# Optimization experiments

Hardware: AMD Instinct MI355X
Metric: run time of the kernel (lower is better)

## Reference

```python
import jax, jax.numpy as jnp
import numpy as np

B, D = 32, 2048


def setup_inputs() -> dict:
    key = jax.random.key(0)
    ks = jax.random.split(key, 7)
    # torch init: weights ~ N(0, 0.1^2); biases default Linear uniform(-1/sqrt(D), 1/sqrt(D))
    bound = 1.0 / np.sqrt(D)
    return {
        "x": jax.random.normal(ks[0], (B, D), dtype=jnp.float32),
        "Wq": 0.1 * jax.random.normal(ks[1], (D, D), dtype=jnp.float32),
        "bq": jax.random.uniform(ks[2], (D,), minval=-bound, maxval=bound, dtype=jnp.float32),
        "Wk": 0.1 * jax.random.normal(ks[3], (D, D), dtype=jnp.float32),
        "bk": jax.random.uniform(ks[4], (D,), minval=-bound, maxval=bound, dtype=jnp.float32),
        "Wv": 0.1 * jax.random.normal(ks[5], (D, D), dtype=jnp.float32),
        "bv": jax.random.uniform(ks[6], (D,), minval=-bound, maxval=bound, dtype=jnp.float32),
    }


def reference(x, Wq, bq, Wk, bk, Wv, bv):
    # q,k,v: [B, D] feature-wise projections (torch Linear: x @ W^T + b)
    q = x @ Wq.T + bq
    k = x @ Wk.T + bk
    v = x @ Wv.T + bv
    # rank-1 outer product scores[b,i,j] = q[b,i] * k[b,j]  -> [B, D, D]
    scores = q[:, :, None] * k[:, None, :]
    # softmax over dim=1 (as in the original F.softmax(..., dim=1))
    weights = jax.nn.softmax(scores, axis=1)
    # weighted V sum: out[b,i] = sum_j weights[b,i,j] * v[b,j]  -> [B, D]
    out = jnp.einsum("bij,bj->bi", weights, v)
    return out
```

## Files before the change

### kernel.cpp

```cpp
#include <hip/hip_runtime.h>
#include <math.h>


#define D 2048
#define BATCH 32
#define CAP 2080
#define WIN8 260

#define Q_OFF   0
#define K2_OFF  65536
#define V_OFF   131072
#define Z_OFF   196608
#define CNT_OFF 262144
#define MM_OFF  262208
#define KDP_OFF 262272
#define XH_OFF  395392
#define XL_OFF  428160

#define L2E 1.4426950408889634f

typedef short s16x8 __attribute__((ext_vector_type(8)));
typedef float f32x4 __attribute__((ext_vector_type(4)));
typedef unsigned short u16;

union FragU { s16x8 v; unsigned u[4]; };

__device__ __forceinline__ float fast_exp2(float x) {
#if __has_builtin(__builtin_amdgcn_exp2f)
  return __builtin_amdgcn_exp2f(x);
#else
  return exp2f(x);
#endif
}
__device__ __forceinline__ u16 f2bf(float f) {
  unsigned u = __float_as_uint(f);
  u = u + 0x7FFFu + ((u >> 16) & 1u);
  return (u16)(u >> 16);
}
__device__ __forceinline__ float bf2f(u16 h) {
  return __uint_as_float(((unsigned)h) << 16);
}
__device__ __forceinline__ void cvt2(float a, float b, unsigned& hp,
                                     unsigned& lp) {
  unsigned ua = __float_as_uint(a), ub = __float_as_uint(b);
  unsigned ha = ua & 0xFFFF0000u, hb = ub & 0xFFFF0000u;
  float la = a - __uint_as_float(ha);
  float lb = b - __uint_as_float(hb);
  hp = (ua >> 16) | hb;
  lp = (__float_as_uint(la) >> 16) | (__float_as_uint(lb) & 0xFFFF0000u);
}

__global__ __launch_bounds__(256) void k0_init(
    const float* __restrict__ x,
    const float* __restrict__ bq, const float* __restrict__ bk,
    const float* __restrict__ bv, float* __restrict__ ws,
    float* __restrict__ out) {
  const int bx = blockIdx.x, tid = threadIdx.x;
  if (bx < 768) {
    const int g = bx * 256 + tid;
    const int m = g >> 16, i = g & 2047;
    ws[g] = (m == 0) ? bq[i] : (m == 1) ? bk[i] * L2E : bv[i];
  } else if (bx < 832) {
    const int idx = (bx - 768) * 256 + tid;
    float4 v = ((const float4*)x)[idx];
    u16* xh = (u16*)(ws + XH_OFF);
    u16* xl = (u16*)(ws + XL_OFF);
    u16 h0 = f2bf(v.x), h1 = f2bf(v.y), h2 = f2bf(v.z), h3 = f2bf(v.w);
    ushort4 hh = {h0, h1, h2, h3};
    ushort4 ll = {f2bf(v.x - bf2f(h0)), f2bf(v.y - bf2f(h1)),
                  f2bf(v.z - bf2f(h2)), f2bf(v.w - bf2f(h3))};
    *(ushort4*)(xh + idx * 4) = hh;
    *(ushort4*)(xl + idx * 4) = ll;
  } else if (bx < 1089) {
    const int g = (bx - 832) * 256 + tid;
    if (g < 65600) ws[Z_OFF + g] = 0.f;
  } else if (bx < 1153) {
    const int idx = (bx - 1089) * 256 + tid;
    ((float4*)out)[idx] = make_float4(0.f, 0.f, 0.f, 0.f);
  } else {
    const int idx = (bx - 1153) * 256 + tid;
    ((float2*)(ws + KDP_OFF))[idx] = make_float2(0.f, -1e30f);
  }
}

__global__ __launch_bounds__(256, 3) void k1_proj(
    const float* __restrict__ Wq, const float* __restrict__ Wk,
    const float* __restrict__ Wv, float* __restrict__ ws) {
  __shared__ float red[4][512];
  const int tid = threadIdx.x;
  const int lane = tid & 63, wv = tid >> 6;
  const int tile = blockIdx.x >> 1, kh = blockIdx.x & 1;
  const int r0 = tile * 16;
  const int m = r0 >> 11, lr = r0 & 2047;
  const float* W = (m == 0) ? Wq : (m == 1) ? Wk : Wv;
  const u16* xh = (const u16*)(ws + XH_OFF);
  const u16* xl = (const u16*)(ws + XL_OFF);

  const int kbase = kh * 1024 + wv * 256 + (lane >> 4) * 8;
  const float* ap = W + (size_t)(lr + (lane & 15)) * D + kbase;
  const u16* bh0 = xh + (size_t)(lane & 15) * D + kbase;
  const u16* bl0 = xl + (size_t)(lane & 15) * D + kbase;
  const u16* bh1 = bh0 + 16 * D;
  const u16* bl1 = bl0 + 16 * D;

  f32x4 acc0 = {0.f, 0.f, 0.f, 0.f}, acc1 = {0.f, 0.f, 0.f, 0.f};
#pragma unroll
  for (int s = 0; s < 8; ++s) {
    float4 fa = *(const float4*)(ap + s * 32);
    float4 fb = *(const float4*)(ap + s * 32 + 4);
    s16x8 Bh0 = *(const s16x8*)(bh0 + s * 32);
    s16x8 Bl0 = *(const s16x8*)(bl0 + s * 32);
    s16x8 Bh1 = *(const s16x8*)(bh1 + s * 32);
    s16x8 Bl1 = *(const s16x8*)(bl1 + s * 32);
    FragU Ah, Al;
    cvt2(fa.x, fa.y, Ah.u[0], Al.u[0]);
    cvt2(fa.z, fa.w, Ah.u[1], Al.u[1]);
    cvt2(fb.x, fb.y, Ah.u[2], Al.u[2]);
    cvt2(fb.z, fb.w, Ah.u[3], Al.u[3]);
    acc0 = __builtin_amdgcn_mfma_f32_16x16x32_bf16(Ah.v, Bh0, acc0, 0, 0, 0);
    acc1 = __builtin_amdgcn_mfma_f32_16x16x32_bf16(Ah.v, Bh1, acc1, 0, 0, 0);
    acc0 = __builtin_amdgcn_mfma_f32_16x16x32_bf16(Ah.v, Bl0, acc0, 0, 0, 0);
    acc1 = __builtin_amdgcn_mfma_f32_16x16x32_bf16(Ah.v, Bl1, acc1, 0, 0, 0);
    acc0 = __builtin_amdgcn_mfma_f32_16x16x32_bf16(Al.v, Bh0, acc0, 0, 0, 0);
    acc1 = __builtin_amdgcn_mfma_f32_16x16x32_bf16(Al.v, Bh1, acc1, 0, 0, 0);
  }
  const int col = lane & 15, rq = (lane >> 4) * 4;
#pragma unroll
  for (int r = 0; r < 4; ++r) {
    red[wv][col * 16 + rq + r] = acc0[r];
    red[wv][(col + 16) * 16 + rq + r] = acc1[r];
  }
  __syncthreads();
  const float scale = (m == 1) ? L2E : 1.0f;
#pragma unroll
  for (int i = tid; i < 512; i += 256) {
    float s = ((red[0][i] + red[1][i]) + (red[2][i] + red[3][i])) * scale;
    atomicAdd(ws + (size_t)m * 65536 + (size_t)(i >> 4) * D + lr + (i & 15), s);
  }
}

__global__ __launch_bounds__(256) void k2_minmax(float* __restrict__ ws) {
  const int b = blockIdx.x, tid = threadIdx.x;
  const float* q = ws + Q_OFF + (size_t)b * D;
  float mx = -1e30f, mn = 1e30f;
  for (int i = tid; i < D / 4; i += 256) {
    float4 v = *(const float4*)(q + i * 4);
    mx = fmaxf(mx, fmaxf(fmaxf(v.x, v.y), fmaxf(v.z, v.w)));
    mn = fminf(mn, fminf(fminf(v.x, v.y), fminf(v.z, v.w)));
  }
#pragma unroll
  for (int off = 32; off; off >>= 1) {
    mx = fmaxf(mx, __shfl_down(mx, off));
    mn = fminf(mn, __shfl_down(mn, off));
  }
  __shared__ float smx[4], smn[4];
  if ((tid & 63) == 0) { smx[tid >> 6] = mx; smn[tid >> 6] = mn; }
  __syncthreads();
  if (tid == 0) {
    mx = fmaxf(fmaxf(smx[0], smx[1]), fmaxf(smx[2], smx[3]));
    mn = fminf(fminf(smn[0], smn[1]), fminf(smn[2], smn[3]));
    ws[MM_OFF + b] = mx;
    ws[MM_OFF + 32 + b] = mn;
  }
}

__global__ __launch_bounds__(256, 8) void k3_denom(float* __restrict__ ws) {
  __shared__ float qs[256];
  const int bx = blockIdx.x, tid = threadIdx.x;
  const int b = bx >> 6, rem = bx & 63, jc = rem >> 3, ih = rem & 7;
  if (tid < 64)
    *(float4*)&qs[tid * 4] =
        *(const float4*)(ws + Q_OFF + (size_t)b * D + ih * 256 + tid * 4);
  __syncthreads();

  const int j = jc * 256 + tid;
  const float k2 = ws[K2_OFF + (size_t)b * D + j];
  const float qmax = ws[MM_OFF + b], qmin = ws[MM_OFF + 32 + b];
  const float m2 = (k2 >= 0.f) ? k2 * qmax : k2 * qmin;
  const float nm2 = -m2;
  float z0 = 0.f, z1 = 0.f, z2 = 0.f, z3 = 0.f;
#pragma unroll 4
  for (int i = 0; i < 256; i += 4) {
    float4 qv = *(const float4*)&qs[i];
    z0 += fast_exp2(fmaf(qv.x, k2, nm2));
    z1 += fast_exp2(fmaf(qv.y, k2, nm2));
    z2 += fast_exp2(fmaf(qv.z, k2, nm2));
    z3 += fast_exp2(fmaf(qv.w, k2, nm2));
  }
  atomicAdd(ws + Z_OFF + (size_t)b * D + j, (z0 + z1) + (z2 + z3));
}

__global__ __launch_bounds__(256) void k3b_finalize(float* __restrict__ ws) {
  const int bx = blockIdx.x;
  const int b = bx >> 3;
  const int j = (bx & 7) * 256 + threadIdx.x;
  const size_t o = (size_t)b * D + j;
  const float k2 = ws[K2_OFF + o];
  const float Z = ws[Z_OFF + o];
  const float v = ws[V_OFF + o];
  const float qmax = ws[MM_OFF + b], qmin = ws[MM_OFF + 32 + b];
  const float m2 = (k2 >= 0.f) ? k2 * qmax : k2 * qmin;
  const float d = __log2f(fabsf(v) / Z) - m2;
  int* cnt = (int*)(ws + CNT_OFF);
  int slot;
  if (v >= 0.f) slot = atomicAdd(&cnt[b], 1);
  else          slot = CAP - 1 - atomicAdd(&cnt[32 + b], 1);
  float2* kdp = (float2*)(ws + KDP_OFF) + (size_t)b * CAP;
  kdp[slot] = make_float2(k2, d);
}

__global__ __launch_bounds__(256, 8) void k4_out(const float* __restrict__ ws,
                                                 float* __restrict__ out) {
  __shared__ float kd[WIN8 * 2];
  const int bx = blockIdx.x, tid = threadIdx.x;
  const int b = bx >> 6, rem = bx & 63, ic = rem >> 3, jw = rem & 7;
  const int w0 = jw * WIN8;
  const float* src = ws + KDP_OFF + (size_t)b * (CAP * 2) + (size_t)w0 * 2;
  if (tid < (WIN8 * 2) / 4)
    *(float4*)&kd[tid * 4] = *(const float4*)(src + tid * 4);
  const int npos = ((const int*)(ws + CNT_OFF))[b];
  __syncthreads();

  const int i = ic * 256 + tid;
  const float qi = ws[Q_OFF + (size_t)b * D + i];

  const int posEnd = (npos + 7) & ~7;
  const int negStart = (CAP - (D - npos)) & ~7;
  int aHi = min(posEnd, w0 + WIN8) - w0; if (aHi < 0) aHi = 0;
  int bLo = max(negStart, w0) - w0;      if (bLo > WIN8) bLo = WIN8;

  float p0 = 0.f, p1 = 0.f, p2 = 0.f, p3 = 0.f;
  for (int jj = 0; jj < aHi; jj += 4) {
    float4 t0 = *(const float4*)&kd[jj * 2];
    float4 t1 = *(const float4*)&kd[jj * 2 + 4];
    p0 += fast_exp2(fmaf(qi, t0.x, t0.y));
    p1 += fast_exp2(fmaf(qi, t0.z, t0.w));
    p2 += fast_exp2(fmaf(qi, t1.x, t1.y));
    p3 += fast_exp2(fmaf(qi, t1.z, t1.w));
  }
  float n0 = 0.f, n1 = 0.f, n2 = 0.f, n3 = 0.f;
  for (int jj = bLo; jj < WIN8; jj += 4) {
    float4 t0 = *(const float4*)&kd[jj * 2];
    float4 t1 = *(const float4*)&kd[jj * 2 + 4];
    n0 += fast_exp2(fmaf(qi, t0.x, t0.y));
    n1 += fast_exp2(fmaf(qi, t0.z, t0.w));
    n2 += fast_exp2(fmaf(qi, t1.x, t1.y));
    n3 += fast_exp2(fmaf(qi, t1.z, t1.w));
  }
  float res = ((p0 + p1) + (p2 + p3)) - ((n0 + n1) + (n2 + n3));
  atomicAdd(out + (size_t)b * D + i, res);
}

extern "C" void kernel_launch(void* const* d_in, const int* in_sizes, int n_in,
                              void* d_out, int out_size, void* d_ws, size_t ws_size,
                              hipStream_t stream) {
  (void)in_sizes; (void)n_in; (void)out_size; (void)ws_size;
  const float* x  = (const float*)d_in[0];
  const float* Wq = (const float*)d_in[1];
  const float* bq = (const float*)d_in[2];
  const float* Wk = (const float*)d_in[3];
  const float* bk = (const float*)d_in[4];
  const float* Wv = (const float*)d_in[5];
  const float* bv = (const float*)d_in[6];
  float* ws  = (float*)d_ws;
  float* out = (float*)d_out;

  k0_init<<<1413, 256, 0, stream>>>(x, bq, bk, bv, ws, out);
  k1_proj<<<768, 256, 0, stream>>>(Wq, Wk, Wv, ws);
  k2_minmax<<<BATCH, 256, 0, stream>>>(ws);
  k3_denom<<<2048, 256, 0, stream>>>(ws);
  k3b_finalize<<<256, 256, 0, stream>>>(ws);
  k4_out<<<2048, 256, 0, stream>>>(ws, out);
}
```

Measured before the change: 159.6 us.

## Fuse minmax, denominator and finalize into one kernel; drop atomics via split partial buffers

The projection now writes its two K-halves into separate partial buffers instead of atomically accumulating onto bias-initialized outputs. Bias add, q min/max, the softmax denominator and the sign-partitioned (k,d) packing are fused into a single per-(batch, j-chunk) kernel that uses block-local counters and per-segment padding. The output kernel processes all 8 segments per block and reduces in shared memory, so out no longer needs zero-init or atomics. This removes several launches, the init kernel's clears and global atomics, at the cost of fewer, larger blocks (256 per kernel) and a full 1024-length q sweep per thread.

```diff
diff --git a/kernel.cpp b/kernel.cpp
--- a/kernel.cpp
+++ b/kernel.cpp
@@ -4,18 +4,14 @@
 
 #define D 2048
 #define BATCH 32
-#define CAP 2080
-#define WIN8 260
-
-#define Q_OFF   0
-#define K2_OFF  65536
-#define V_OFF   131072
-#define Z_OFF   196608
-#define CNT_OFF 262144
-#define MM_OFF  262208
-#define KDP_OFF 262272
-#define XH_OFF  395392
-#define XL_OFF  428160
+#define SEG 260
+
+#define XH_OFF  0
+#define XL_OFF  32768
+#define PA_OFF  65536
+#define PB_OFF  262144
+#define KDP_OFF 458752
+#define NP_OFF  591872
 
 #define L2E 1.4426950408889634f
 
@@ -50,37 +46,18 @@
   lp = (__float_as_uint(la) >> 16) | (__float_as_uint(lb) & 0xFFFF0000u);
 }
 
-__global__ __launch_bounds__(256) void k0_init(
-    const float* __restrict__ x,
-    const float* __restrict__ bq, const float* __restrict__ bk,
-    const float* __restrict__ bv, float* __restrict__ ws,
-    float* __restrict__ out) {
-  const int bx = blockIdx.x, tid = threadIdx.x;
-  if (bx < 768) {
-    const int g = bx * 256 + tid;
-    const int m = g >> 16, i = g & 2047;
-    ws[g] = (m == 0) ? bq[i] : (m == 1) ? bk[i] * L2E : bv[i];
-  } else if (bx < 832) {
-    const int idx = (bx - 768) * 256 + tid;
-    float4 v = ((const float4*)x)[idx];
-    u16* xh = (u16*)(ws + XH_OFF);
-    u16* xl = (u16*)(ws + XL_OFF);
-    u16 h0 = f2bf(v.x), h1 = f2bf(v.y), h2 = f2bf(v.z), h3 = f2bf(v.w);
-    ushort4 hh = {h0, h1, h2, h3};
-    ushort4 ll = {f2bf(v.x - bf2f(h0)), f2bf(v.y - bf2f(h1)),
-                  f2bf(v.z - bf2f(h2)), f2bf(v.w - bf2f(h3))};
-    *(ushort4*)(xh + idx * 4) = hh;
-    *(ushort4*)(xl + idx * 4) = ll;
-  } else if (bx < 1089) {
-    const int g = (bx - 832) * 256 + tid;
-    if (g < 65600) ws[Z_OFF + g] = 0.f;
-  } else if (bx < 1153) {
-    const int idx = (bx - 1089) * 256 + tid;
-    ((float4*)out)[idx] = make_float4(0.f, 0.f, 0.f, 0.f);
-  } else {
-    const int idx = (bx - 1153) * 256 + tid;
-    ((float2*)(ws + KDP_OFF))[idx] = make_float2(0.f, -1e30f);
-  }
+__global__ __launch_bounds__(64) void k0_cvt(const float* __restrict__ x,
+                                             float* __restrict__ ws) {
+  const int idx = blockIdx.x * 64 + threadIdx.x;
+  float4 v = ((const float4*)x)[idx];
+  u16* xh = (u16*)(ws + XH_OFF);
+  u16* xl = (u16*)(ws + XL_OFF);
+  u16 h0 = f2bf(v.x), h1 = f2bf(v.y), h2 = f2bf(v.z), h3 = f2bf(v.w);
+  ushort4 hh = {h0, h1, h2, h3};
+  ushort4 ll = {f2bf(v.x - bf2f(h0)), f2bf(v.y - bf2f(h1)),
+                f2bf(v.z - bf2f(h2)), f2bf(v.w - bf2f(h3))};
+  *(ushort4*)(xh + idx * 4) = hh;
+  *(ushort4*)(xl + idx * 4) = ll;
 }
 
 __global__ __launch_bounds__(256, 3) void k1_proj(
@@ -131,124 +108,136 @@
     red[wv][(col + 16) * 16 + rq + r] = acc1[r];
   }
   __syncthreads();
-  const float scale = (m == 1) ? L2E : 1.0f;
+  float* part = ws + (kh ? PB_OFF : PA_OFF) + (size_t)m * 65536;
 #pragma unroll
   for (int i = tid; i < 512; i += 256) {
-    float s = ((red[0][i] + red[1][i]) + (red[2][i] + red[3][i])) * scale;
-    atomicAdd(ws + (size_t)m * 65536 + (size_t)(i >> 4) * D + lr + (i & 15), s);
-  }
-}
-
-__global__ __launch_bounds__(256) void k2_minmax(float* __restrict__ ws) {
-  const int b = blockIdx.x, tid = threadIdx.x;
-  const float* q = ws + Q_OFF + (size_t)b * D;
-  float mx = -1e30f, mn = 1e30f;
-  for (int i = tid; i < D / 4; i += 256) {
-    float4 v = *(const float4*)(q + i * 4);
-    mx = fmaxf(mx, fmaxf(fmaxf(v.x, v.y), fmaxf(v.z, v.w)));
-    mn = fminf(mn, fminf(fminf(v.x, v.y), fminf(v.z, v.w)));
-  }
+    float s = (red[0][i] + red[1][i]) + (red[2][i] + red[3][i]);
+    part[(size_t)(i >> 4) * D + lr + (i & 15)] = s;
+  }
+}
+
+__global__ __launch_bounds__(512) void k3_dz(float* __restrict__ ws,
+                                             const float* __restrict__ bq,
+                                             const float* __restrict__ bk,
+                                             const float* __restrict__ bv) {
+  __shared__ float qs[2048];
+  __shared__ float zs[512];
+  __shared__ float rmx[8], rmn[8];
+  __shared__ int cnt[2];
+  const int bx = blockIdx.x, t = threadIdx.x;
+  const int b = bx >> 3, jc = bx & 7;
+  if (t == 0) { cnt[0] = 0; cnt[1] = 0; }
+
+  const float* qA = ws + PA_OFF + (size_t)b * D;
+  const float* qB = ws + PB_OFF + (size_t)b * D;
+  float4 a4 = ((const float4*)qA)[t];
+  float4 b4 = ((const float4*)qB)[t];
+  float4 c4 = ((const float4*)bq)[t];
+  float4 qv = {a4.x + b4.x + c4.x, a4.y + b4.y + c4.y,
+               a4.z + b4.z + c4.z, a4.w + b4.w + c4.w};
+  *(float4*)&qs[t * 4] = qv;
+  float mx = fmaxf(fmaxf(qv.x, qv.y), fmaxf(qv.z, qv.w));
+  float mn = fminf(fminf(qv.x, qv.y), fminf(qv.z, qv.w));
 #pragma unroll
   for (int off = 32; off; off >>= 1) {
     mx = fmaxf(mx, __shfl_down(mx, off));
     mn = fminf(mn, __shfl_down(mn, off));
   }
-  __shared__ float smx[4], smn[4];
-  if ((tid & 63) == 0) { smx[tid >> 6] = mx; smn[tid >> 6] = mn; }
-  __syncthreads();
-  if (tid == 0) {
-    mx = fmaxf(fmaxf(smx[0], smx[1]), fmaxf(smx[2], smx[3]));
-    mn = fminf(fminf(smn[0], smn[1]), fminf(smn[2], smn[3]));
-    ws[MM_OFF + b] = mx;
-    ws[MM_OFF + 32 + b] = mn;
-  }
-}
-
-__global__ __launch_bounds__(256, 8) void k3_denom(float* __restrict__ ws) {
-  __shared__ float qs[256];
-  const int bx = blockIdx.x, tid = threadIdx.x;
-  const int b = bx >> 6, rem = bx & 63, jc = rem >> 3, ih = rem & 7;
-  if (tid < 64)
-    *(float4*)&qs[tid * 4] =
-        *(const float4*)(ws + Q_OFF + (size_t)b * D + ih * 256 + tid * 4);
-  __syncthreads();
-
-  const int j = jc * 256 + tid;
-  const float k2 = ws[K2_OFF + (size_t)b * D + j];
-  const float qmax = ws[MM_OFF + b], qmin = ws[MM_OFF + 32 + b];
-  const float m2 = (k2 >= 0.f) ? k2 * qmax : k2 * qmin;
+  if ((t & 63) == 0) { rmx[t >> 6] = mx; rmn[t >> 6] = mn; }
+  __syncthreads();
+  mx = rmx[0]; mn = rmn[0];
+#pragma unroll
+  for (int w = 1; w < 8; ++w) {
+    mx = fmaxf(mx, rmx[w]);
+    mn = fminf(mn, rmn[w]);
+  }
+
+  const int jl = t & 255, ih = t >> 8;
+  const size_t jo = (size_t)b * D + jc * 256 + jl;
+  const float k2 =
+      (ws[PA_OFF + 65536 + jo] + ws[PB_OFF + 65536 + jo] + bk[jc * 256 + jl]) *
+      L2E;
+  const float m2 = (k2 >= 0.f) ? k2 * mx : k2 * mn;
   const float nm2 = -m2;
+  const float* qp = qs + ih * 1024;
   float z0 = 0.f, z1 = 0.f, z2 = 0.f, z3 = 0.f;
 #pragma unroll 4
-  for (int i = 0; i < 256; i += 4) {
-    float4 qv = *(const float4*)&qs[i];
-    z0 += fast_exp2(fmaf(qv.x, k2, nm2));
-    z1 += fast_exp2(fmaf(qv.y, k2, nm2));
-    z2 += fast_exp2(fmaf(qv.z, k2, nm2));
-    z3 += fast_exp2(fmaf(qv.w, k2, nm2));
-  }
-  atomicAdd(ws + Z_OFF + (size_t)b * D + j, (z0 + z1) + (z2 + z3));
-}
-
-__global__ __launch_bounds__(256) void k3b_finalize(float* __restrict__ ws) {
-  const int bx = blockIdx.x;
-  const int b = bx >> 3;
-  const int j = (bx & 7) * 256 + threadIdx.x;
-  const size_t o = (size_t)b * D + j;
-  const float k2 = ws[K2_OFF + o];
-  const float Z = ws[Z_OFF + o];
-  const float v = ws[V_OFF + o];
-  const float qmax = ws[MM_OFF + b], qmin = ws[MM_OFF + 32 + b];
-  const float m2 = (k2 >= 0.f) ? k2 * qmax : k2 * qmin;
-  const float d = __log2f(fabsf(v) / Z) - m2;
-  int* cnt = (int*)(ws + CNT_OFF);
-  int slot;
-  if (v >= 0.f) slot = atomicAdd(&cnt[b], 1);
-  else          slot = CAP - 1 - atomicAdd(&cnt[32 + b], 1);
-  float2* kdp = (float2*)(ws + KDP_OFF) + (size_t)b * CAP;
-  kdp[slot] = make_float2(k2, d);
-}
-
-__global__ __launch_bounds__(256, 8) void k4_out(const float* __restrict__ ws,
-                                                 float* __restrict__ out) {
-  __shared__ float kd[WIN8 * 2];
-  const int bx = blockIdx.x, tid = threadIdx.x;
-  const int b = bx >> 6, rem = bx & 63, ic = rem >> 3, jw = rem & 7;
-  const int w0 = jw * WIN8;
-  const float* src = ws + KDP_OFF + (size_t)b * (CAP * 2) + (size_t)w0 * 2;
-  if (tid < (WIN8 * 2) / 4)
-    *(float4*)&kd[tid * 4] = *(const float4*)(src + tid * 4);
-  const int npos = ((const int*)(ws + CNT_OFF))[b];
-  __syncthreads();
-
-  const int i = ic * 256 + tid;
-  const float qi = ws[Q_OFF + (size_t)b * D + i];
-
-  const int posEnd = (npos + 7) & ~7;
-  const int negStart = (CAP - (D - npos)) & ~7;
-  int aHi = min(posEnd, w0 + WIN8) - w0; if (aHi < 0) aHi = 0;
-  int bLo = max(negStart, w0) - w0;      if (bLo > WIN8) bLo = WIN8;
+  for (int i = 0; i < 1024; i += 4) {
+    float4 q4 = *(const float4*)&qp[i];
+    z0 += fast_exp2(fmaf(q4.x, k2, nm2));
+    z1 += fast_exp2(fmaf(q4.y, k2, nm2));
+    z2 += fast_exp2(fmaf(q4.z, k2, nm2));
+    z3 += fast_exp2(fmaf(q4.w, k2, nm2));
+  }
+  zs[t] = (z0 + z1) + (z2 + z3);
+  __syncthreads();
+
+  float2* kdp = (float2*)(ws + KDP_OFF) + ((size_t)b * 8 + jc) * SEG;
+  if (t < 256) {
+    float Z = zs[t] + zs[t + 256];
+    float v =
+        ws[PA_OFF + 131072 + jo] + ws[PB_OFF + 131072 + jo] + bv[jc * 256 + jl];
+    float d = __log2f(fabsf(v) / Z) - m2;
+    int slot;
+    if (v >= 0.f) slot = atomicAdd(&cnt[0], 1);
+    else          slot = (SEG - 1) - atomicAdd(&cnt[1], 1);
+    kdp[slot] = make_float2(k2, d);
+  }
+  __syncthreads();
+  const int npos = cnt[0];
+  if (t < 4) kdp[npos + t] = make_float2(0.f, -1e30f);
+  if (t == 0) ((int*)(ws + NP_OFF))[b * 8 + jc] = npos;
+}
+
+__global__ __launch_bounds__(512) void k4_out(const float* __restrict__ ws,
+                                              const float* __restrict__ bq,
+                                              float* __restrict__ out) {
+  __shared__ float2 kd[8 * SEG];
+  __shared__ int np[8];
+  __shared__ float rs[512];
+  const int bx = blockIdx.x, t = threadIdx.x;
+  const int b = bx >> 3, ic = bx & 7;
+
+  const float4* src = (const float4*)((const float2*)(ws + KDP_OFF) +
+                                      (size_t)b * 8 * SEG);
+  for (int idx = t; idx < (8 * SEG) / 2; idx += 512)
+    ((float4*)kd)[idx] = src[idx];
+  if (t < 8) np[t] = ((const int*)(ws + NP_OFF))[b * 8 + t];
+
+  const int il = t & 255, jh = t >> 8;
+  const int i = ic * 256 + il;
+  const size_t io = (size_t)b * D + i;
+  const float qi = ws[PA_OFF + io] + ws[PB_OFF + io] + bq[i];
+  __syncthreads();
 
   float p0 = 0.f, p1 = 0.f, p2 = 0.f, p3 = 0.f;
-  for (int jj = 0; jj < aHi; jj += 4) {
-    float4 t0 = *(const float4*)&kd[jj * 2];
-    float4 t1 = *(const float4*)&kd[jj * 2 + 4];
-    p0 += fast_exp2(fmaf(qi, t0.x, t0.y));
-    p1 += fast_exp2(fmaf(qi, t0.z, t0.w));
-    p2 += fast_exp2(fmaf(qi, t1.x, t1.y));
-    p3 += fast_exp2(fmaf(qi, t1.z, t1.w));
-  }
   float n0 = 0.f, n1 = 0.f, n2 = 0.f, n3 = 0.f;
-  for (int jj = bLo; jj < WIN8; jj += 4) {
-    float4 t0 = *(const float4*)&kd[jj * 2];
-    float4 t1 = *(const float4*)&kd[jj * 2 + 4];
-    n0 += fast_exp2(fmaf(qi, t0.x, t0.y));
-    n1 += fast_exp2(fmaf(qi, t0.z, t0.w));
-    n2 += fast_exp2(fmaf(qi, t1.x, t1.y));
-    n3 += fast_exp2(fmaf(qi, t1.z, t1.w));
-  }
-  float res = ((p0 + p1) + (p2 + p3)) - ((n0 + n1) + (n2 + n3));
-  atomicAdd(out + (size_t)b * D + i, res);
+#pragma unroll
+  for (int s = jh * 4; s < jh * 4 + 4; ++s) {
+    const float2* seg = kd + s * SEG;
+    const int npos = np[s];
+    const int pe = (npos + 3) & ~3;
+    const int ns = (npos + 4) & ~3;
+    for (int jj = 0; jj < pe; jj += 4) {
+      float4 t0 = *(const float4*)&seg[jj];
+      float4 t1 = *(const float4*)&seg[jj + 2];
+      p0 += fast_exp2(fmaf(qi, t0.x, t0.y));
+      p1 += fast_exp2(fmaf(qi, t0.z, t0.w));
+      p2 += fast_exp2(fmaf(qi, t1.x, t1.y));
+      p3 += fast_exp2(fmaf(qi, t1.z, t1.w));
+    }
+    for (int jj = ns; jj < SEG; jj += 4) {
+      float4 t0 = *(const float4*)&seg[jj];
+      float4 t1 = *(const float4*)&seg[jj + 2];
+      n0 += fast_exp2(fmaf(qi, t0.x, t0.y));
+      n1 += fast_exp2(fmaf(qi, t0.z, t0.w));
+      n2 += fast_exp2(fmaf(qi, t1.x, t1.y));
+      n3 += fast_exp2(fmaf(qi, t1.z, t1.w));
+    }
+  }
+  rs[t] = ((p0 + p1) + (p2 + p3)) - ((n0 + n1) + (n2 + n3));
+  __syncthreads();
+  if (t < 256) out[io] = rs[t] + rs[t + 256];
 }
 
 extern "C" void kernel_launch(void* const* d_in, const int* in_sizes, int n_in,
@@ -265,10 +254,8 @@
   float* ws  = (float*)d_ws;
   float* out = (float*)d_out;
 
-  k0_init<<<1413, 256, 0, stream>>>(x, bq, bk, bv, ws, out);
+  k0_cvt<<<256, 64, 0, stream>>>(x, ws);
   k1_proj<<<768, 256, 0, stream>>>(Wq, Wk, Wv, ws);
-  k2_minmax<<<BATCH, 256, 0, stream>>>(ws);
-  k3_denom<<<2048, 256, 0, stream>>>(ws);
-  k3b_finalize<<<256, 256, 0, stream>>>(ws);
-  k4_out<<<2048, 256, 0, stream>>>(ws, out);
-}
+  k3_dz<<<256, 512, 0, stream>>>(ws, bq, bk, bv);
+  k4_out<<<256, 512, 0, stream>>>(ws, bq, out);
+}
```

Result: faster. 151.7 us (-4.9%).
